# Kernel tuning notes

Hardware: AMD Instinct MI355X
Metric: run time of the kernel (lower is better)

## Reference

```python
import jax, jax.numpy as jnp
import numpy as np

K = 20  # neighbors


def _knn(x, k):
    # x: (B, C, N) -> (B, N, k) indices of k nearest neighbors (max of negative sq dist)
    inner = -2.0 * jnp.einsum('bcn,bcm->bnm', x, x)
    xx = jnp.sum(x * x, axis=1)  # (B, N)
    pd = -xx[:, :, None] - inner - xx[:, None, :]  # (B, N, N)
    return jax.lax.top_k(pd, k)[1]


def _graph_feature(x, k, dim9=False):
    # x: (B, C, N) -> (B, 2C, N, k) edge features [x_j - x_i, x_i]
    idx = _knn(x[:, 6:] if dim9 else x, k)  # (B, N, k)
    xt = jnp.transpose(x, (0, 2, 1))  # (B, N, C)
    nbr = jax.vmap(lambda t, i: t[i])(xt, idx)  # (B, N, k, C) gather
    ctr = jnp.broadcast_to(xt[:, :, None, :], nbr.shape)
    f = jnp.concatenate([nbr - ctr, ctr], axis=-1)  # (B, N, k, 2C)
    return jnp.transpose(f, (0, 3, 1, 2))


def _bn(y, p, nd):
    # inference-mode batchnorm; p = stacked (gamma, beta, mean, var) of shape (4, C)
    g, b, m, v = p
    shp = (1, -1) + (1,) * nd
    return (y - m.reshape(shp)) * (g.reshape(shp) / jnp.sqrt(v.reshape(shp) + 1e-5)) + b.reshape(shp)


def _cbr2(x, W, p):  # 1x1 conv2d + BN2d + LeakyReLU(0.2)
    return jax.nn.leaky_relu(_bn(jnp.einsum('oc,bcnk->bonk', W, x), p, 2), 0.2)


def _cbr1(x, W, p):  # 1x1 conv1d + BN1d + LeakyReLU(0.2)
    return jax.nn.leaky_relu(_bn(jnp.einsum('oc,bcn->bon', W, x), p, 1), 0.2)


def _forward(x, W1, W2, W3, W4, W5, W6, W7, W8, W9, bn1, bn2, bn3, bn4, bn5, bn6, bn7, bn8):
    N = x.shape[2]
    h = _graph_feature(x, K, dim9=True)          # (B, 12, N, K)
    h = _cbr2(h, W1, bn1)
    h = _cbr2(h, W2, bn2)
    x1 = jnp.max(h, axis=-1)                     # (B, 64, N)
    h = _graph_feature(x1, K)                    # (B, 128, N, K)
    h = _cbr2(h, W3, bn3)
    h = _cbr2(h, W4, bn4)
    x2 = jnp.max(h, axis=-1)
    h = _graph_feature(x2, K)
    h = _cbr2(h, W5, bn5)
    x3 = jnp.max(h, axis=-1)
    h = jnp.concatenate([x1, x2, x3], axis=1)    # (B, 192, N)
    h = _cbr1(h, W6, bn6)                        # (B, 1024, N)
    g = jnp.max(h, axis=-1, keepdims=True)       # global feature
    g = jnp.broadcast_to(g, (g.shape[0], g.shape[1], N))
    h = jnp.concatenate([g, x1, x2, x3], axis=1) # (B, 1216, N)
    h = _cbr1(h, W7, bn7)
    h = _cbr1(h, W8, bn8)                        # dropout is identity in eval
    return jnp.einsum('oc,bcn->bon', W9, h)      # (B, 13, N) logits


def setup_inputs() -> dict:
    key = jax.random.key(0)
    ks = jax.random.split(key, 20)
    B, C, N = 4, 6, 4096

    def w(k, o, c):
        return jax.random.normal(k, (o, c), jnp.float32) * (1.0 / np.sqrt(c))

    def bn(k, c):
        k1, k2, k3, k4 = jax.random.split(k, 4)
        g = jax.random.uniform(k1, (c,), jnp.float32, 0.5, 1.5)
        b = jax.random.normal(k2, (c,), jnp.float32) * 0.1
        m = jax.random.normal(k3, (c,), jnp.float32) * 0.1
        v = jax.random.uniform(k4, (c,), jnp.float32, 0.5, 1.5)
        return jnp.stack([g, b, m, v])

    return {
        'x': jax.random.normal(ks[0], (B, C, N), jnp.float32),
        'W1': w(ks[1], 64, 12), 'W2': w(ks[2], 64, 64), 'W3': w(ks[3], 64, 128),
        'W4': w(ks[4], 64, 64), 'W5': w(ks[5], 64, 128), 'W6': w(ks[6], 1024, 192),
        'W7': w(ks[7], 512, 1216), 'W8': w(ks[8], 256, 512), 'W9': w(ks[9], 13, 256),
        'bn1': bn(ks[10], 64), 'bn2': bn(ks[11], 64), 'bn3': bn(ks[12], 64),
        'bn4': bn(ks[13], 64), 'bn5': bn(ks[14], 64), 'bn6': bn(ks[15], 1024),
        'bn7': bn(ks[16], 512), 'bn8': bn(ks[17], 256),
    }


def reference(x, W1, W2, W3, W4, W5, W6, W7, W8, W9, bn1, bn2, bn3, bn4, bn5, bn6, bn7, bn8):
    return _forward(x, W1, W2, W3, W4, W5, W6, W7, W8, W9,
                    bn1, bn2, bn3, bn4, bn5, bn6, bn7, bn8)
```

## Files before the change

kernel.cpp:

```cpp
#include <hip/hip_runtime.h>
#include <math.h>

#define N_PTS 4096
#define BATCH 4
#define KNB 20

typedef __attribute__((ext_vector_type(8))) short short8v;
typedef __attribute__((ext_vector_type(4))) float f32x4;

__device__ __forceinline__ float lrelu(float v){ return fmaxf(v, 0.2f*v); }
__device__ __forceinline__ unsigned fenc(float f){ unsigned u=__float_as_uint(f); return (u&0x80000000u)?~u:(u|0x80000000u); }
__device__ __forceinline__ float fdec(unsigned k){ return (k&0x80000000u)?__uint_as_float(k&0x7fffffffu):__uint_as_float(~k); }

__device__ __forceinline__ unsigned pack2(float v){
  unsigned u = __float_as_uint(v);
  unsigned hi = (u + 0x7fffu + ((u>>16)&1u)) >> 16;
  float hf = __uint_as_float(hi<<16);
  unsigned u2 = __float_as_uint(v - hf);
  unsigned lo = (u2 + 0x7fffu + ((u2>>16)&1u)) >> 16;
  return (hi<<16) | lo;
}
__device__ __forceinline__ void cvt8(uint4 v0, uint4 v1, short8v& h, short8v& l){
  unsigned a0=v0.x,a1=v0.y,a2=v0.z,a3=v0.w,a4=v1.x,a5=v1.y,a6=v1.z,a7=v1.w;
  h[0]=(short)(a0>>16); l[0]=(short)(a0&0xffffu);
  h[1]=(short)(a1>>16); l[1]=(short)(a1&0xffffu);
  h[2]=(short)(a2>>16); l[2]=(short)(a2&0xffffu);
  h[3]=(short)(a3>>16); l[3]=(short)(a3&0xffffu);
  h[4]=(short)(a4>>16); l[4]=(short)(a4&0xffffu);
  h[5]=(short)(a5>>16); l[5]=(short)(a5&0xffffu);
  h[6]=(short)(a6>>16); l[6]=(short)(a6&0xffffu);
  h[7]=(short)(a7>>16); l[7]=(short)(a7&0xffffu);
}

__global__ void k_scale_rows(const float* __restrict__ W, const float* __restrict__ bn,
                             float* __restrict__ Wf, float* __restrict__ bias, int O, int C){
  int i = blockIdx.x*256 + threadIdx.x;
  if (i >= O*C) return;
  int o = i / C;
  float s = bn[o] / sqrtf(bn[3*O+o] + 1e-5f);
  Wf[i] = W[i]*s;
  if (i % C == 0) bias[o] = bn[O+o] - s*bn[2*O+o];
}

__global__ void k_pack_w(const float* __restrict__ W, int ldw, int c0,
                         const float* __restrict__ bn, int O, int C, int Opad,
                         unsigned* __restrict__ out, float* __restrict__ bias){
  int i = blockIdx.x*256 + threadIdx.x;
  if (i >= Opad*C) return;
  int o = i / C, c = i - o*C;
  float v = 0.f;
  if (o < O){
    float s = 1.f;
    if (bn != nullptr){
      s = bn[o] / sqrtf(bn[3*O+o] + 1e-5f);
      if (bias != nullptr && c == 0) bias[o] = bn[O+o] - s*bn[2*O+o];
    }
    v = W[o*ldw + c0 + c] * s;
  }
  out[i] = pack2(v);
}

__global__ void k_build_T4(const float* __restrict__ W, int ldw, const float* __restrict__ bn,
                           float* __restrict__ dst, float* __restrict__ bias,
                           int c0, int diffoff, int Csrc){
  int o = threadIdx.x, c = blockIdx.x;
  float s = bn[o] / sqrtf(bn[192+o] + 1e-5f);
  float val = 0.f;
  if (c < Csrc){
    val = W[o*ldw + c0 + c];
    if (diffoff) val = W[o*ldw + c0 + diffoff + c] - val;
    val *= s;
  }
  dst[(c>>2)*256 + o*4 + (c&3)] = val;
  if (bias != nullptr && c==0) bias[o] = bn[64+o] - s*bn[128+o];
}

__global__ void k_build_U1(const float* __restrict__ x, const float* __restrict__ W1,
                           const float* __restrict__ bn, float* __restrict__ U1){
  int o = threadIdx.x, k = blockIdx.x, b = blockIdx.y;
  float s = bn[o] / sqrtf(bn[192+o] + 1e-5f);
  float acc = 0.f;
  #pragma unroll
  for (int c=0;c<6;c++) acc += W1[o*12+c] * x[(b*6+c)*N_PTS + k];
  U1[(b*KNB+k)*64 + o] = acc*s;
}

__global__ void k_init_g(unsigned* g){ g[blockIdx.x*256+threadIdx.x] = fenc(-INFINITY); }

__global__ __launch_bounds__(256) void k_edge1(const float* __restrict__ x, const float* __restrict__ U1,
                        const float* __restrict__ W1dT4, const float* __restrict__ bf1,
                        const float* __restrict__ W2T4, const float* __restrict__ bf2,
                        float* __restrict__ x1t, unsigned* __restrict__ Xb, float* __restrict__ xx1){
  __shared__ float hb[4][KNB][64];
  int wid = threadIdx.x>>6, lane = threadIdx.x&63;
  int pt = blockIdx.x*4 + wid, b = pt>>12, n = pt&4095;
  float xv[8];
  #pragma unroll
  for (int c=0;c<6;c++) xv[c] = x[(b*6+c)*N_PTS + n];
  xv[6]=0.f; xv[7]=0.f;
  float w = bf1[lane];
  #pragma unroll
  for (int cb=0;cb<2;cb++){
    float4 wv = ((const float4*)W1dT4)[cb*64+lane];
    w = fmaf(wv.x, xv[cb*4+0], w); w = fmaf(wv.y, xv[cb*4+1], w);
    w = fmaf(wv.z, xv[cb*4+2], w); w = fmaf(wv.w, xv[cb*4+3], w);
  }
  const float* Ub = U1 + b*KNB*64;
  #pragma unroll
  for (int k=0;k<KNB;k++) hb[wid][k][lane] = lrelu(Ub[k*64+lane] + w);
  __syncthreads();
  float acc[KNB];
  #pragma unroll
  for (int k=0;k<KNB;k++) acc[k] = bf2[lane];
  for (int cb=0;cb<16;cb++){
    float4 wv = ((const float4*)W2T4)[cb*64+lane];
    #pragma unroll
    for (int k=0;k<KNB;k++){
      float4 a = *(const float4*)&hb[wid][k][cb*4];
      acc[k]=fmaf(wv.x,a.x,acc[k]); acc[k]=fmaf(wv.y,a.y,acc[k]);
      acc[k]=fmaf(wv.z,a.z,acc[k]); acc[k]=fmaf(wv.w,a.w,acc[k]);
    }
  }
  float mx = -INFINITY;
  #pragma unroll
  for (int k=0;k<KNB;k++) mx = fmaxf(mx, acc[k]);
  mx = lrelu(mx);
  x1t[(size_t)pt*64 + lane] = mx;
  Xb[((size_t)((b<<12)+n))*192 + 0 + lane] = pack2(mx);
  float sq = mx*mx;
  #pragma unroll
  for (int off=32; off; off>>=1) sq += __shfl_xor(sq, off);
  if (lane==0) xx1[pt] = sq;
}

__global__ __launch_bounds__(256) void k_uv(const float* __restrict__ xt, const float* __restrict__ WL,
    const float* __restrict__ WRd, const float* __restrict__ bf,
    float* __restrict__ Ut, float* __restrict__ Vt){
  __shared__ float xs[4][64];
  int wid = threadIdx.x>>6, lane = threadIdx.x&63;
  int pt = blockIdx.x*4 + wid;
  xs[wid][lane] = xt[(size_t)pt*64 + lane];
  __syncthreads();
  float U = 0.f, V = bf[lane];
  #pragma unroll
  for (int cb=0;cb<16;cb++){
    float4 wl = ((const float4*)WL)[cb*64+lane];
    float4 wr = ((const float4*)WRd)[cb*64+lane];
    float4 xv = *(const float4*)&xs[wid][cb*4];
    U=fmaf(wl.x,xv.x,U); U=fmaf(wl.y,xv.y,U); U=fmaf(wl.z,xv.z,U); U=fmaf(wl.w,xv.w,U);
    V=fmaf(wr.x,xv.x,V); V=fmaf(wr.y,xv.y,V); V=fmaf(wr.z,xv.z,V); V=fmaf(wr.w,xv.w,V);
  }
  Ut[(size_t)pt*64 + lane] = U;
  Vt[(size_t)pt*64 + lane] = V;
}

__global__ __launch_bounds__(256) void k_ec2(const float* __restrict__ Ut, const float* __restrict__ Vt,
    const int* __restrict__ idx, const float* __restrict__ W2T4, const float* __restrict__ bfb,
    float* __restrict__ xout, unsigned* __restrict__ Xb, float* __restrict__ xxout){
  __shared__ float H[4][KNB][64];
  int wid = threadIdx.x>>6, lane = threadIdx.x&63;
  int pt = blockIdx.x*4 + wid, b = pt>>12, n = pt&4095;
  const float* Ub = Ut + (((size_t)b)<<12)*64;
  float Vv = Vt[(size_t)pt*64 + lane];
  int mr[KNB];
  const int4* ip4 = (const int4*)(idx + (size_t)pt*KNB);
  #pragma unroll
  for (int q=0;q<5;q++){ int4 t = ip4[q]; mr[q*4+0]=t.x; mr[q*4+1]=t.y; mr[q*4+2]=t.z; mr[q*4+3]=t.w; }
  #pragma unroll
  for (int k=0;k<KNB;k++) H[wid][k][lane] = lrelu(Ub[(size_t)mr[k]*64 + lane] + Vv);
  __syncthreads();
  float acc[KNB];
  #pragma unroll
  for (int k=0;k<KNB;k++) acc[k] = bfb[lane];
  for (int cb=0;cb<16;cb++){
    float4 wv = ((const float4*)W2T4)[cb*64+lane];
    #pragma unroll
    for (int k=0;k<KNB;k++){
      float4 a = *(const float4*)&H[wid][k][cb*4];
      acc[k]=fmaf(wv.x,a.x,acc[k]); acc[k]=fmaf(wv.y,a.y,acc[k]);
      acc[k]=fmaf(wv.z,a.z,acc[k]); acc[k]=fmaf(wv.w,a.w,acc[k]);
    }
  }
  float mx = -INFINITY;
  #pragma unroll
  for (int k=0;k<KNB;k++) mx = fmaxf(mx, acc[k]);
  mx = lrelu(mx);
  xout[(size_t)pt*64 + lane] = mx;
  Xb[((size_t)((b<<12)+n))*192 + 64 + lane] = pack2(mx);
  float sq = mx*mx;
  #pragma unroll
  for (int off=32;off;off>>=1) sq += __shfl_xor(sq,off);
  if (lane==0) xxout[pt] = sq;
}

__global__ __launch_bounds__(256) void k_ec3(const float* __restrict__ Ut, const float* __restrict__ Vt,
    const int* __restrict__ idx, unsigned* __restrict__ Xb){
  int wid = threadIdx.x>>6, lane = threadIdx.x&63;
  int pt = blockIdx.x*4 + wid, b = pt>>12, n = pt&4095;
  const float* Ub = Ut + (((size_t)b)<<12)*64;
  int mr[KNB];
  const int4* ip4 = (const int4*)(idx + (size_t)pt*KNB);
  #pragma unroll
  for (int q=0;q<5;q++){ int4 t = ip4[q]; mr[q*4+0]=t.x; mr[q*4+1]=t.y; mr[q*4+2]=t.z; mr[q*4+3]=t.w; }
  float mx = -INFINITY;
  #pragma unroll
  for (int k=0;k<KNB;k++) mx = fmaxf(mx, Ub[(size_t)mr[k]*64 + lane]);
  mx = lrelu(mx + Vt[(size_t)pt*64 + lane]);
  Xb[((size_t)((b<<12)+n))*192 + 128 + lane] = pack2(mx);
}

__global__ __launch_bounds__(512) void k_knn_mfma(const unsigned* __restrict__ Xp, int coff,
        const float* __restrict__ xx, unsigned* __restrict__ pd, unsigned* __restrict__ cmax,
        int q0, int S){
  __shared__ short Ah[128][40];
  __shared__ short Al[128][40];
  __shared__ short Bh[128][40];
  __shared__ short Bl[128][40];
  int tid = threadIdx.x;
  int bx = blockIdx.x, by = blockIdx.y, bz = blockIdx.z;
  int w = tid>>6, lane = tid&63;
  int r15 = lane&15, rb = lane>>4;
  int mibase = (w&3)*32, oibase = (w>>2)*64;
  f32x4 acc[2][4];
  #pragma unroll
  for (int mi=0;mi<2;mi++)
    #pragma unroll
    for (int oi=0;oi<4;oi++) acc[mi][oi] = (f32x4){0.f,0.f,0.f,0.f};
  int srow = tid>>2, sc = (tid&3)*8;
  const unsigned* pa = Xp + ((size_t)((bz<<12) + q0 + by*128 + srow))*192 + coff + sc;
  const unsigned* pb = Xp + ((size_t)((bz<<12) + bx*128 + srow))*192 + coff + sc;
  for (int kt=0; kt<64; kt+=32){
    if (kt) __syncthreads();
    uint4 a0 = *(const uint4*)(pa+kt);
    uint4 a1 = *(const uint4*)(pa+kt+4);
    uint4 b0 = *(const uint4*)(pb+kt);
    uint4 b1 = *(const uint4*)(pb+kt+4);
    short8v h, l;
    cvt8(a0,a1,h,l);
    *(short8v*)&Ah[srow][sc] = h; *(short8v*)&Al[srow][sc] = l;
    cvt8(b0,b1,h,l);
    *(short8v*)&Bh[srow][sc] = h; *(short8v*)&Bl[srow][sc] = l;
    __syncthreads();
    short8v ah[2], al[2];
    #pragma unroll
    for (int mi=0;mi<2;mi++){
      ah[mi] = *(const short8v*)&Ah[mibase+mi*16+r15][rb*8];
      al[mi] = *(const short8v*)&Al[mibase+mi*16+r15][rb*8];
    }
    #pragma unroll
    for (int oi=0;oi<4;oi++){
      short8v bh = *(const short8v*)&Bh[oibase+oi*16+r15][rb*8];
      short8v bl = *(const short8v*)&Bl[oibase+oi*16+r15][rb*8];
      #pragma unroll
      for (int mi=0;mi<2;mi++){
        acc[mi][oi] = __builtin_amdgcn_mfma_f32_16x16x32_bf16(ah[mi], bh, acc[mi][oi], 0,0,0);
        acc[mi][oi] = __builtin_amdgcn_mfma_f32_16x16x32_bf16(ah[mi], bl, acc[mi][oi], 0,0,0);
        acc[mi][oi] = __builtin_amdgcn_mfma_f32_16x16x32_bf16(al[mi], bh, acc[mi][oi], 0,0,0);
      }
    }
  }
  float xm[4];
  #pragma unroll
  for (int oi=0;oi<4;oi++) xm[oi] = xx[(bz<<12) + bx*128 + oibase + oi*16 + r15];
  #pragma unroll
  for (int mi=0;mi<2;mi++){
    #pragma unroll
    for (int r=0;r<4;r++){
      int row = by*128 + mibase + mi*16 + rb*4 + r;
      float xn = xx[(bz<<12) + q0 + row];
      float f0 = fmaf(2.f, acc[mi][0][r], -xn) - xm[0];
      float f1 = fmaf(2.f, acc[mi][1][r], -xn) - xm[1];
      float f2 = fmaf(2.f, acc[mi][2][r], -xn) - xm[2];
      float f3 = fmaf(2.f, acc[mi][3][r], -xn) - xm[3];
      unsigned* dst = pd + ((size_t)(bz*S + row))*N_PTS + bx*128 + oibase;
      dst[ 0+r15] = fenc(f0);
      dst[16+r15] = fenc(f1);
      dst[32+r15] = fenc(f2);
      dst[48+r15] = fenc(f3);
      float m = fmaxf(fmaxf(f0,f1), fmaxf(f2,f3));
      m = fmaxf(m, __shfl_xor(m,1));
      m = fmaxf(m, __shfl_xor(m,2));
      m = fmaxf(m, __shfl_xor(m,4));
      m = fmaxf(m, __shfl_xor(m,8));
      if (r15 == 0)
        cmax[((size_t)(bz<<12) + q0 + row)*64 + bx*2 + (oibase>>6)] = fenc(m);
    }
  }
}

__device__ __forceinline__ unsigned bitsort_u32(unsigned v, int lane){
  #pragma unroll
  for (int k=2;k<=64;k<<=1){
    #pragma unroll
    for (int j=k>>1;j>0;j>>=1){
      unsigned o = (unsigned)__shfl_xor((int)v, j);
      bool takeMax = (((lane & j) != 0) == ((lane & k) == 0));
      unsigned mx = v>o?v:o, mn = v<o?v:o;
      v = takeMax ? mx : mn;
    }
  }
  return v;
}

__global__ __launch_bounds__(256,4) void k_topk20(const unsigned* __restrict__ pdbuf,
        const unsigned* __restrict__ cmax, int* __restrict__ idxout, int q0, int sshift){
  __shared__ unsigned long long cand[4][64];
  int wid = threadIdx.x>>6, lane = threadIdx.x&63;
  int gw = blockIdx.x*4 + wid;
  int S = 1 << sshift;
  int b = gw >> sshift, i = gw & (S-1);
  const unsigned* row = pdbuf + ((size_t)b*S + i)*N_PTS;
  unsigned cm = cmax[((size_t)b*N_PTS + q0 + i)*64 + lane];
  unsigned T = (unsigned)__shfl((int)bitsort_u32(cm, lane), 44);
  unsigned long long qual = __ballot(cm >= T);
  unsigned lmax = 0u;
  for (int c=0;c<64;c++){
    if (!((qual>>c)&1ull)) continue;
    unsigned vv = row[c*64 + lane];
    lmax = lmax > vv ? lmax : vv;
  }
  unsigned T2 = (unsigned)__shfl((int)bitsort_u32(lmax, lane), 44);
  int base = 0;
  unsigned long long below = (1ull<<lane) - 1ull;
  for (int c=0;c<64;c++){
    if (!((qual>>c)&1ull)) continue;
    unsigned vv = row[c*64 + lane];
    bool isc = vv >= T2;
    unsigned long long mb = __ballot(isc);
    int pos = base + __popcll(mb & below);
    if (isc && pos < 64){
      int m = c*64 + lane;
      cand[wid][pos] = (((unsigned long long)vv)<<12) | (unsigned)(4095-m);
    }
    base += __popcll(mb);
  }
  unsigned long long K;
  if (base <= 64){
    unsigned long long kv = (lane < base) ? cand[wid][lane] : 0ull;
    #pragma unroll
    for (int k=2;k<=64;k<<=1){
      #pragma unroll
      for (int j=k>>1;j>0;j>>=1){
        unsigned long long o = __shfl_xor(kv, j);
        bool takeMax = (((lane & j) != 0) == ((lane & k) == 0));
        unsigned long long mx = kv>o?kv:o, mn = kv<o?kv:o;
        kv = takeMax ? mx : mn;
      }
    }
    K = __shfl(kv, 44);
  } else {
    K = 0ull;
    for (int bb2=43; bb2>=0; --bb2){
      unsigned long long cnd = K | (1ull<<bb2);
      int lc = 0;
      for (int c=0;c<64;c++){
        if (!((qual>>c)&1ull)) continue;
        unsigned vv = row[c*64 + lane];
        int m = c*64 + lane;
        unsigned long long key = (((unsigned long long)vv)<<12) | (unsigned)(4095-m);
        if (key >= cnd) lc++;
      }
      #pragma unroll
      for (int off=32; off; off>>=1) lc += __shfl_xor(lc, off);
      if (lc >= KNB) K = cnd;
    }
  }
  int eb = 0;
  int* dst = idxout + ((size_t)b*N_PTS + (q0+i))*KNB;
  for (int c=0;c<64;c++){
    if (!((qual>>c)&1ull)) continue;
    unsigned vv = row[c*64 + lane];
    int m = c*64 + lane;
    unsigned long long key = (((unsigned long long)vv)<<12) | (unsigned)(4095-m);
    bool sel = key >= K;
    unsigned long long mb = __ballot(sel);
    int pos = eb + __popcll(mb & below);
    if (sel) dst[pos] = m;
    eb += __popcll(mb);
  }
}

template<int STORE, int RELU>
__global__ __launch_bounds__(512) void k_mgemm(const unsigned* __restrict__ Ap, int lda,
        const unsigned* __restrict__ Bp, int ldb,
        const float* __restrict__ bias, int perBatch,
        unsigned* __restrict__ Cp, int ldo, float* __restrict__ Cf,
        unsigned* __restrict__ gmax, int O, int K){
  __shared__ short Ah[128][40];
  __shared__ short Al[128][40];
  __shared__ short Bh[128][40];
  __shared__ short Bl[128][40];
  int tid = threadIdx.x;
  int bx = blockIdx.x, by = blockIdx.y, bz = blockIdx.z;
  int w = tid>>6, lane = tid&63;
  int r15 = lane&15, rb = lane>>4;
  int mibase = (w&3)*32, oibase = (w>>2)*64;
  f32x4 acc[2][4];
  #pragma unroll
  for (int mi=0;mi<2;mi++)
    #pragma unroll
    for (int oi=0;oi<4;oi++) acc[mi][oi] = (f32x4){0.f,0.f,0.f,0.f};
  int srow = tid>>2, sc = (tid&3)*8;
  const unsigned* pa = Ap + ((size_t)((bz<<12) + bx*128 + srow))*lda + sc;
  const unsigned* pb = Bp + (size_t)(by*128 + srow)*ldb + sc;
  for (int kt=0; kt<K; kt+=32){
    if (kt) __syncthreads();
    uint4 a0 = *(const uint4*)(pa+kt);
    uint4 a1 = *(const uint4*)(pa+kt+4);
    uint4 b0 = *(const uint4*)(pb+kt);
    uint4 b1 = *(const uint4*)(pb+kt+4);
    short8v h, l;
    cvt8(a0,a1,h,l);
    *(short8v*)&Ah[srow][sc] = h; *(short8v*)&Al[srow][sc] = l;
    cvt8(b0,b1,h,l);
    *(short8v*)&Bh[srow][sc] = h; *(short8v*)&Bl[srow][sc] = l;
    __syncthreads();
    short8v ah[2], al[2];
    #pragma unroll
    for (int mi=0;mi<2;mi++){
      ah[mi] = *(const short8v*)&Ah[mibase+mi*16+r15][rb*8];
      al[mi] = *(const short8v*)&Al[mibase+mi*16+r15][rb*8];
    }
    #pragma unroll
    for (int oi=0;oi<4;oi++){
      short8v bh = *(const short8v*)&Bh[oibase+oi*16+r15][rb*8];
      short8v bl = *(const short8v*)&Bl[oibase+oi*16+r15][rb*8];
      #pragma unroll
      for (int mi=0;mi<2;mi++){
        acc[mi][oi] = __builtin_amdgcn_mfma_f32_16x16x32_bf16(ah[mi], bh, acc[mi][oi], 0,0,0);
        acc[mi][oi] = __builtin_amdgcn_mfma_f32_16x16x32_bf16(ah[mi], bl, acc[mi][oi], 0,0,0);
        acc[mi][oi] = __builtin_amdgcn_mfma_f32_16x16x32_bf16(al[mi], bh, acc[mi][oi], 0,0,0);
      }
    }
  }
  #pragma unroll
  for (int oi=0;oi<4;oi++){
    int o = by*128 + oibase + oi*16 + r15;
    float bv = 0.f;
    if (bias != nullptr) bv = perBatch ? bias[bz*O + o] : bias[o];
    float cmx = -INFINITY;
    #pragma unroll
    for (int mi=0;mi<2;mi++){
      #pragma unroll
      for (int r=0;r<4;r++){
        float y = acc[mi][oi][r] + bv;
        if (RELU) y = lrelu(y);
        if (STORE==1){
          int pt = bx*128 + mibase + mi*16 + rb*4 + r;
          Cp[((size_t)((bz<<12)+pt))*ldo + o] = pack2(y);
        } else if (STORE==2){
          if (o < 13){
            int pt = bx*128 + mibase + mi*16 + rb*4 + r;
            Cf[(((size_t)(bz*13 + o))<<12) + pt] = y;
          }
        } else {
          cmx = fmaxf(cmx, y);
        }
      }
    }
    if (STORE==0){
      cmx = fmaxf(cmx, __shfl_xor(cmx,16));
      cmx = fmaxf(cmx, __shfl_xor(cmx,32));
      if (rb==0) atomicMax(&gmax[bz*1024 + o], fenc(cmx));
    }
  }
}

__global__ __launch_bounds__(256) void k_gemv7(const float* __restrict__ Wf7, const float* __restrict__ bf7,
                        const unsigned* __restrict__ g, float* __restrict__ bias7){
  int wid = threadIdx.x>>6, lane = threadIdx.x&63;
  int o = blockIdx.x*4 + wid, b = blockIdx.y;
  const float* wr = Wf7 + (size_t)o*1216;
  const unsigned* gb = g + b*1024;
  float acc = 0.f;
  for (int c = lane; c < 1024; c += 64)
    acc = fmaf(wr[c], fdec(gb[c]), acc);
  #pragma unroll
  for (int off=32; off; off>>=1) acc += __shfl_xor(acc, off);
  if (lane==0) bias7[b*512+o] = acc + bf7[o];
}

extern "C" void kernel_launch(void* const* d_in, const int* in_sizes, int n_in,
                              void* d_out, int out_size, void* d_ws, size_t ws_size,
                              hipStream_t stream){
  const float* x  = (const float*)d_in[0];
  const float* W1 = (const float*)d_in[1];
  const float* W2 = (const float*)d_in[2];
  const float* W3 = (const float*)d_in[3];
  const float* W4 = (const float*)d_in[4];
  const float* W5 = (const float*)d_in[5];
  const float* W6 = (const float*)d_in[6];
  const float* W7 = (const float*)d_in[7];
  const float* W8 = (const float*)d_in[8];
  const float* W9 = (const float*)d_in[9];
  const float* bn1 = (const float*)d_in[10];
  const float* bn2 = (const float*)d_in[11];
  const float* bn3 = (const float*)d_in[12];
  const float* bn4 = (const float*)d_in[13];
  const float* bn5 = (const float*)d_in[14];
  const float* bn6 = (const float*)d_in[15];
  const float* bn7 = (const float*)d_in[16];
  const float* bn8 = (const float*)d_in[17];

  float* ws = (float*)d_ws;
  size_t off = 0;
  auto alloc = [&](size_t nf){ float* p = ws + off; off += (nf + 63) & ~(size_t)63; return p; };
  float* Wf7 = alloc((size_t)512*1216); float* bf7 = alloc(512);
  float* bf6 = alloc(1024);
  float* bf8 = alloc(256);
  unsigned* Wb6p = (unsigned*)alloc((size_t)1024*192);
  unsigned* Wb7p = (unsigned*)alloc((size_t)512*192);
  unsigned* Wb8p = (unsigned*)alloc((size_t)256*512);
  unsigned* Wb9p = (unsigned*)alloc((size_t)128*256);
  float* W1dT4 = alloc(8*64);     float* bf1 = alloc(64);
  float* W2T4  = alloc(64*64);    float* bf2 = alloc(64);
  float* W3LT4 = alloc(64*64);    float* W3RdT4 = alloc(64*64); float* bf3 = alloc(64);
  float* W4T4  = alloc(64*64);    float* bf4 = alloc(64);
  float* W5LT4 = alloc(64*64);    float* W5RdT4 = alloc(64*64); float* bf5 = alloc(64);
  float* U1  = alloc(4*KNB*64);
  float* x1t = alloc((size_t)4*N_PTS*64);
  float* x2t = alloc((size_t)4*N_PTS*64);
  float* Ut3 = alloc((size_t)4*N_PTS*64);
  float* Vt3 = alloc((size_t)4*N_PTS*64);
  float* Ut5 = alloc((size_t)4*N_PTS*64);
  float* Vt5 = alloc((size_t)4*N_PTS*64);
  unsigned* Xb = (unsigned*)alloc((size_t)4*N_PTS*192);
  float* xx1 = alloc(4*N_PTS);
  float* xx2 = alloc(4*N_PTS);
  int* idx1 = (int*)alloc((size_t)4*N_PTS*KNB);
  int* idx2 = (int*)alloc((size_t)4*N_PTS*KNB);
  unsigned* genc = (unsigned*)alloc(4*1024);
  float* bias7 = alloc(4*512);
  unsigned* h8p = (unsigned*)alloc((size_t)4*N_PTS*256);
  unsigned* cmaxb = (unsigned*)alloc((size_t)4*N_PTS*64);
  size_t remaining = (ws_size / 4 > off) ? (ws_size / 4 - off) : 0;
  int S = 4096;
  while (S > 512 && (size_t)4*S*N_PTS + 1024 > remaining) S >>= 1;
  if (S > 1024) S = 1024;
  int sshift = 31 - __builtin_clz(S);
  unsigned* pdbuf = (unsigned*)alloc((size_t)4*S*N_PTS);
  unsigned* h7p = pdbuf;

  k_scale_rows<<<(512*1216+255)/256,256,0,stream>>>(W7, bn7, Wf7, bf7, 512, 1216);
  k_pack_w<<<(1024*192+255)/256,256,0,stream>>>(W6, 192, 0, bn6, 1024, 192, 1024, Wb6p, bf6);
  k_pack_w<<<(512*192+255)/256,256,0,stream>>>(W7, 1216, 1024, bn7, 512, 192, 512, Wb7p, nullptr);
  k_pack_w<<<(256*512+255)/256,256,0,stream>>>(W8, 512, 0, bn8, 256, 512, 256, Wb8p, bf8);
  k_pack_w<<<(128*256+255)/256,256,0,stream>>>(W9, 256, 0, nullptr, 13, 256, 128, Wb9p, nullptr);
  k_build_T4<<<8,64,0,stream>>>(W1, 12, bn1, W1dT4, bf1, 0, 6, 6);
  k_build_T4<<<64,64,0,stream>>>(W2, 64, bn2, W2T4, bf2, 0, 0, 64);
  k_build_T4<<<64,64,0,stream>>>(W3, 128, bn3, W3LT4, bf3, 0, 0, 64);
  k_build_T4<<<64,64,0,stream>>>(W3, 128, bn3, W3RdT4, nullptr, 0, 64, 64);
  k_build_T4<<<64,64,0,stream>>>(W4, 64, bn4, W4T4, bf4, 0, 0, 64);
  k_build_T4<<<64,64,0,stream>>>(W5, 128, bn5, W5LT4, bf5, 0, 0, 64);
  k_build_T4<<<64,64,0,stream>>>(W5, 128, bn5, W5RdT4, nullptr, 0, 64, 64);
  k_build_U1<<<dim3(KNB,4),64,0,stream>>>(x, W1, bn1, U1);
  k_init_g<<<16,256,0,stream>>>(genc);

  k_edge1<<<4096,256,0,stream>>>(x, U1, W1dT4, bf1, W2T4, bf2, x1t, Xb, xx1);

  int nstripe = N_PTS / S;
  for (int s=0;s<nstripe;s++){
    k_knn_mfma<<<dim3(32,S/128,4),512,0,stream>>>(Xb, 0, xx1, pdbuf, cmaxb, s*S, S);
    k_topk20<<<S,256,0,stream>>>(pdbuf, cmaxb, idx1, s*S, sshift);
  }

  k_uv<<<4096,256,0,stream>>>(x1t, W3LT4, W3RdT4, bf3, Ut3, Vt3);
  k_ec2<<<4096,256,0,stream>>>(Ut3, Vt3, idx1, W4T4, bf4, x2t, Xb, xx2);

  for (int s=0;s<nstripe;s++){
    k_knn_mfma<<<dim3(32,S/128,4),512,0,stream>>>(Xb, 64, xx2, pdbuf, cmaxb, s*S, S);
    k_topk20<<<S,256,0,stream>>>(pdbuf, cmaxb, idx2, s*S, sshift);
  }

  k_uv<<<4096,256,0,stream>>>(x2t, W5LT4, W5RdT4, bf5, Ut5, Vt5);
  k_ec3<<<4096,256,0,stream>>>(Ut5, Vt5, idx2, Xb);

  k_mgemm<0,1><<<dim3(32,8,4),512,0,stream>>>(Xb, 192, Wb6p, 192, bf6, 0, nullptr, 0, nullptr, genc, 1024, 192);
  k_gemv7<<<dim3(128,4),256,0,stream>>>(Wf7, bf7, genc, bias7);
  k_mgemm<1,1><<<dim3(32,4,4),512,0,stream>>>(Xb, 192, Wb7p, 192, bias7, 1, h7p, 512, nullptr, nullptr, 512, 192);
  k_mgemm<1,1><<<dim3(32,2,4),512,0,stream>>>(h7p, 512, Wb8p, 512, bf8, 0, h8p, 256, nullptr, nullptr, 256, 512);
  k_mgemm<2,0><<<dim3(32,1,4),512,0,stream>>>(h8p, 256, Wb9p, 256, nullptr, 0, nullptr, 0, (float*)d_out, nullptr, 13, 256);
}
```

Before: 616.5 us.

## Replace scalar edge-conv 64x64 GEMMs with split-bf16 MFMA kernel

Replaces the scalar-FMA edge-conv kernels for layers 1-2 and 3-4 with one templated kernel. It computes the second 64x64 conv through bf16 hi/lo split MFMA instructions, double-buffering the per-neighbor hidden tile in shared memory and keeping a running max. Layer 1 now precomputes a per-point V1 term in a separate kernel and uses pre-packed W2 and W4 weights. This trades the heavy FP32 FMA loops for matrix-core work, at the cost of extra split-precision MFMAs, one more launch, and a new V1 buffer. The grid is also much smaller, 256 blocks instead of 4096.

```diff
diff --git a/kernel.cpp b/kernel.cpp
--- a/kernel.cpp
+++ b/kernel.cpp
@@ -85,53 +85,20 @@
   U1[(b*KNB+k)*64 + o] = acc*s;
 }
 
+__global__ __launch_bounds__(256) void k_v1(const float* __restrict__ x, const float* __restrict__ W1,
+        const float* __restrict__ bn, float* __restrict__ V1){
+  int o = threadIdx.x&63;
+  int pt = blockIdx.x*4 + (threadIdx.x>>6);
+  int b = pt>>12, n = pt&4095;
+  float s = bn[o] / sqrtf(bn[192+o] + 1e-5f);
+  float acc = bn[64+o] - s*bn[128+o];
+  #pragma unroll
+  for (int c=0;c<6;c++)
+    acc += s*(W1[o*12+6+c]-W1[o*12+c]) * x[(b*6+c)*N_PTS + n];
+  V1[(size_t)pt*64 + o] = acc;
+}
+
 __global__ void k_init_g(unsigned* g){ g[blockIdx.x*256+threadIdx.x] = fenc(-INFINITY); }
-
-__global__ __launch_bounds__(256) void k_edge1(const float* __restrict__ x, const float* __restrict__ U1,
-                        const float* __restrict__ W1dT4, const float* __restrict__ bf1,
-                        const float* __restrict__ W2T4, const float* __restrict__ bf2,
-                        float* __restrict__ x1t, unsigned* __restrict__ Xb, float* __restrict__ xx1){
-  __shared__ float hb[4][KNB][64];
-  int wid = threadIdx.x>>6, lane = threadIdx.x&63;
-  int pt = blockIdx.x*4 + wid, b = pt>>12, n = pt&4095;
-  float xv[8];
-  #pragma unroll
-  for (int c=0;c<6;c++) xv[c] = x[(b*6+c)*N_PTS + n];
-  xv[6]=0.f; xv[7]=0.f;
-  float w = bf1[lane];
-  #pragma unroll
-  for (int cb=0;cb<2;cb++){
-    float4 wv = ((const float4*)W1dT4)[cb*64+lane];
-    w = fmaf(wv.x, xv[cb*4+0], w); w = fmaf(wv.y, xv[cb*4+1], w);
-    w = fmaf(wv.z, xv[cb*4+2], w); w = fmaf(wv.w, xv[cb*4+3], w);
-  }
-  const float* Ub = U1 + b*KNB*64;
-  #pragma unroll
-  for (int k=0;k<KNB;k++) hb[wid][k][lane] = lrelu(Ub[k*64+lane] + w);
-  __syncthreads();
-  float acc[KNB];
-  #pragma unroll
-  for (int k=0;k<KNB;k++) acc[k] = bf2[lane];
-  for (int cb=0;cb<16;cb++){
-    float4 wv = ((const float4*)W2T4)[cb*64+lane];
-    #pragma unroll
-    for (int k=0;k<KNB;k++){
-      float4 a = *(const float4*)&hb[wid][k][cb*4];
-      acc[k]=fmaf(wv.x,a.x,acc[k]); acc[k]=fmaf(wv.y,a.y,acc[k]);
-      acc[k]=fmaf(wv.z,a.z,acc[k]); acc[k]=fmaf(wv.w,a.w,acc[k]);
-    }
-  }
-  float mx = -INFINITY;
-  #pragma unroll
-  for (int k=0;k<KNB;k++) mx = fmaxf(mx, acc[k]);
-  mx = lrelu(mx);
-  x1t[(size_t)pt*64 + lane] = mx;
-  Xb[((size_t)((b<<12)+n))*192 + 0 + lane] = pack2(mx);
-  float sq = mx*mx;
-  #pragma unroll
-  for (int off=32; off; off>>=1) sq += __shfl_xor(sq, off);
-  if (lane==0) xx1[pt] = sq;
-}
 
 __global__ __launch_bounds__(256) void k_uv(const float* __restrict__ xt, const float* __restrict__ WL,
     const float* __restrict__ WRd, const float* __restrict__ bf,
@@ -154,43 +121,121 @@
   Vt[(size_t)pt*64 + lane] = V;
 }
 
-__global__ __launch_bounds__(256) void k_ec2(const float* __restrict__ Ut, const float* __restrict__ Vt,
-    const int* __restrict__ idx, const float* __restrict__ W2T4, const float* __restrict__ bfb,
-    float* __restrict__ xout, unsigned* __restrict__ Xb, float* __restrict__ xxout){
-  __shared__ float H[4][KNB][64];
-  int wid = threadIdx.x>>6, lane = threadIdx.x&63;
-  int pt = blockIdx.x*4 + wid, b = pt>>12, n = pt&4095;
-  const float* Ub = Ut + (((size_t)b)<<12)*64;
-  float Vv = Vt[(size_t)pt*64 + lane];
+template<int GATHER>
+__global__ __launch_bounds__(256) void k_edgemm(const float* __restrict__ Ut,
+    const float* __restrict__ Vt, const int* __restrict__ idx,
+    const unsigned* __restrict__ Wp, const float* __restrict__ bf,
+    float* __restrict__ xout, unsigned* __restrict__ Xb, int coff,
+    float* __restrict__ xxout){
+  __shared__ short Hh[2][64][72];
+  __shared__ short Hl[2][64][72];
+  int tid = threadIdx.x;
+  int b = blockIdx.z, p0 = blockIdx.x*64;
+  int w = tid>>6, lane = tid&63, r15 = lane&15, rb = lane>>4;
+  int ptl = tid>>2, c0 = (tid&3)*16;
+  size_t ptg = ((size_t)b<<12) + p0 + ptl;
+  float v[16];
+  #pragma unroll
+  for (int q=0;q<4;q++){
+    float4 t = *(const float4*)&Vt[ptg*64 + c0 + q*4];
+    v[q*4+0]=t.x; v[q*4+1]=t.y; v[q*4+2]=t.z; v[q*4+3]=t.w;
+  }
   int mr[KNB];
-  const int4* ip4 = (const int4*)(idx + (size_t)pt*KNB);
-  #pragma unroll
-  for (int q=0;q<5;q++){ int4 t = ip4[q]; mr[q*4+0]=t.x; mr[q*4+1]=t.y; mr[q*4+2]=t.z; mr[q*4+3]=t.w; }
-  #pragma unroll
-  for (int k=0;k<KNB;k++) H[wid][k][lane] = lrelu(Ub[(size_t)mr[k]*64 + lane] + Vv);
-  __syncthreads();
-  float acc[KNB];
-  #pragma unroll
-  for (int k=0;k<KNB;k++) acc[k] = bfb[lane];
-  for (int cb=0;cb<16;cb++){
-    float4 wv = ((const float4*)W2T4)[cb*64+lane];
-    #pragma unroll
-    for (int k=0;k<KNB;k++){
-      float4 a = *(const float4*)&H[wid][k][cb*4];
-      acc[k]=fmaf(wv.x,a.x,acc[k]); acc[k]=fmaf(wv.y,a.y,acc[k]);
-      acc[k]=fmaf(wv.z,a.z,acc[k]); acc[k]=fmaf(wv.w,a.w,acc[k]);
-    }
-  }
-  float mx = -INFINITY;
-  #pragma unroll
-  for (int k=0;k<KNB;k++) mx = fmaxf(mx, acc[k]);
-  mx = lrelu(mx);
-  xout[(size_t)pt*64 + lane] = mx;
-  Xb[((size_t)((b<<12)+n))*192 + 64 + lane] = pack2(mx);
-  float sq = mx*mx;
-  #pragma unroll
-  for (int off=32;off;off>>=1) sq += __shfl_xor(sq,off);
-  if (lane==0) xxout[pt] = sq;
+  if (GATHER){
+    const int4* ip4 = (const int4*)(idx + ptg*KNB);
+    #pragma unroll
+    for (int q=0;q<5;q++){ int4 t=ip4[q]; mr[q*4+0]=t.x; mr[q*4+1]=t.y; mr[q*4+2]=t.z; mr[q*4+3]=t.w; }
+  }
+  short8v wh[4][2], wl[4][2];
+  #pragma unroll
+  for (int oi=0;oi<4;oi++)
+    #pragma unroll
+    for (int ks=0;ks<2;ks++){
+      const unsigned* pw = Wp + (size_t)(oi*16+r15)*64 + ks*32 + rb*8;
+      uint4 w0 = *(const uint4*)pw, w1 = *(const uint4*)(pw+4);
+      cvt8(w0,w1,wh[oi][ks],wl[oi][ks]);
+    }
+  f32x4 rmax[4];
+  #pragma unroll
+  for (int oi=0;oi<4;oi++) rmax[oi]=(f32x4){-INFINITY,-INFINITY,-INFINITY,-INFINITY};
+  float uc[16], un[16];
+  {
+    const float* ur = GATHER ? (Ut + ((((size_t)b)<<12) + mr[0])*64 + c0)
+                             : (Ut + ((size_t)b*KNB + 0)*64 + c0);
+    #pragma unroll
+    for (int q=0;q<4;q++){
+      float4 t = *(const float4*)(ur + q*4);
+      uc[q*4+0]=t.x; uc[q*4+1]=t.y; uc[q*4+2]=t.z; uc[q*4+3]=t.w;
+    }
+  }
+  for (int k=0;k<KNB;k++){
+    int buf = k&1;
+    #pragma unroll
+    for (int q=0;q<2;q++){
+      short8v hh, hl;
+      #pragma unroll
+      for (int e=0;e<8;e++){
+        unsigned pk = pack2(lrelu(uc[q*8+e] + v[q*8+e]));
+        hh[e]=(short)(pk>>16); hl[e]=(short)(pk&0xffffu);
+      }
+      *(short8v*)&Hh[buf][ptl][c0+q*8] = hh;
+      *(short8v*)&Hl[buf][ptl][c0+q*8] = hl;
+    }
+    if (k+1 < KNB){
+      const float* ur = GATHER ? (Ut + ((((size_t)b)<<12) + mr[k+1])*64 + c0)
+                               : (Ut + ((size_t)b*KNB + (k+1))*64 + c0);
+      #pragma unroll
+      for (int q=0;q<4;q++){
+        float4 t = *(const float4*)(ur + q*4);
+        un[q*4+0]=t.x; un[q*4+1]=t.y; un[q*4+2]=t.z; un[q*4+3]=t.w;
+      }
+    }
+    __syncthreads();
+    f32x4 acc[4];
+    #pragma unroll
+    for (int oi=0;oi<4;oi++) acc[oi]=(f32x4){0.f,0.f,0.f,0.f};
+    #pragma unroll
+    for (int ks=0;ks<2;ks++){
+      short8v ah = *(const short8v*)&Hh[buf][w*16+r15][ks*32+rb*8];
+      short8v al = *(const short8v*)&Hl[buf][w*16+r15][ks*32+rb*8];
+      #pragma unroll
+      for (int oi=0;oi<4;oi++){
+        acc[oi] = __builtin_amdgcn_mfma_f32_16x16x32_bf16(ah, wh[oi][ks], acc[oi], 0,0,0);
+        acc[oi] = __builtin_amdgcn_mfma_f32_16x16x32_bf16(ah, wl[oi][ks], acc[oi], 0,0,0);
+        acc[oi] = __builtin_amdgcn_mfma_f32_16x16x32_bf16(al, wh[oi][ks], acc[oi], 0,0,0);
+      }
+    }
+    #pragma unroll
+    for (int oi=0;oi<4;oi++)
+      #pragma unroll
+      for (int r=0;r<4;r++) rmax[oi][r] = fmaxf(rmax[oi][r], acc[oi][r]);
+    if (k+1 < KNB){
+      #pragma unroll
+      for (int e=0;e<16;e++) uc[e]=un[e];
+    }
+  }
+  float xs[4] = {0.f,0.f,0.f,0.f};
+  #pragma unroll
+  for (int oi=0;oi<4;oi++){
+    int o = oi*16 + r15;
+    float bv = bf[o];
+    #pragma unroll
+    for (int r=0;r<4;r++){
+      float y = lrelu(rmax[oi][r] + bv);
+      size_t pg = ((size_t)b<<12) + p0 + w*16 + rb*4 + r;
+      if (xout) xout[pg*64 + o] = y;
+      Xb[pg*192 + coff + o] = pack2(y);
+      xs[r] += y*y;
+    }
+  }
+  if (xxout){
+    #pragma unroll
+    for (int r=0;r<4;r++){
+      float s = xs[r];
+      s += __shfl_xor(s,1); s += __shfl_xor(s,2); s += __shfl_xor(s,4); s += __shfl_xor(s,8);
+      if (r15==0) xxout[((size_t)b<<12) + p0 + w*16 + rb*4 + r] = s;
+    }
+  }
 }
 
 __global__ __launch_bounds__(256) void k_ec3(const float* __restrict__ Ut, const float* __restrict__ Vt,
@@ -508,16 +553,18 @@
   float* Wf7 = alloc((size_t)512*1216); float* bf7 = alloc(512);
   float* bf6 = alloc(1024);
   float* bf8 = alloc(256);
+  float* bf2 = alloc(64);
+  float* bf4 = alloc(64);
+  unsigned* Wb2p = (unsigned*)alloc((size_t)64*64);
+  unsigned* Wb4p = (unsigned*)alloc((size_t)64*64);
   unsigned* Wb6p = (unsigned*)alloc((size_t)1024*192);
   unsigned* Wb7p = (unsigned*)alloc((size_t)512*192);
   unsigned* Wb8p = (unsigned*)alloc((size_t)256*512);
   unsigned* Wb9p = (unsigned*)alloc((size_t)128*256);
-  float* W1dT4 = alloc(8*64);     float* bf1 = alloc(64);
-  float* W2T4  = alloc(64*64);    float* bf2 = alloc(64);
   float* W3LT4 = alloc(64*64);    float* W3RdT4 = alloc(64*64); float* bf3 = alloc(64);
-  float* W4T4  = alloc(64*64);    float* bf4 = alloc(64);
   float* W5LT4 = alloc(64*64);    float* W5RdT4 = alloc(64*64); float* bf5 = alloc(64);
   float* U1  = alloc(4*KNB*64);
+  float* V1  = alloc((size_t)4*N_PTS*64);
   float* x1t = alloc((size_t)4*N_PTS*64);
   float* x2t = alloc((size_t)4*N_PTS*64);
   float* Ut3 = alloc((size_t)4*N_PTS*64);
@@ -542,21 +589,21 @@
   unsigned* h7p = pdbuf;
 
   k_scale_rows<<<(512*1216+255)/256,256,0,stream>>>(W7, bn7, Wf7, bf7, 512, 1216);
+  k_pack_w<<<(64*64+255)/256,256,0,stream>>>(W2, 64, 0, bn2, 64, 64, 64, Wb2p, bf2);
+  k_pack_w<<<(64*64+255)/256,256,0,stream>>>(W4, 64, 0, bn4, 64, 64, 64, Wb4p, bf4);
   k_pack_w<<<(1024*192+255)/256,256,0,stream>>>(W6, 192, 0, bn6, 1024, 192, 1024, Wb6p, bf6);
   k_pack_w<<<(512*192+255)/256,256,0,stream>>>(W7, 1216, 1024, bn7, 512, 192, 512, Wb7p, nullptr);
   k_pack_w<<<(256*512+255)/256,256,0,stream>>>(W8, 512, 0, bn8, 256, 512, 256, Wb8p, bf8);
   k_pack_w<<<(128*256+255)/256,256,0,stream>>>(W9, 256, 0, nullptr, 13, 256, 128, Wb9p, nullptr);
-  k_build_T4<<<8,64,0,stream>>>(W1, 12, bn1, W1dT4, bf1, 0, 6, 6);
-  k_build_T4<<<64,64,0,stream>>>(W2, 64, bn2, W2T4, bf2, 0, 0, 64);
   k_build_T4<<<64,64,0,stream>>>(W3, 128, bn3, W3LT4, bf3, 0, 0, 64);
   k_build_T4<<<64,64,0,stream>>>(W3, 128, bn3, W3RdT4, nullptr, 0, 64, 64);
-  k_build_T4<<<64,64,0,stream>>>(W4, 64, bn4, W4T4, bf4, 0, 0, 64);
   k_build_T4<<<64,64,0,stream>>>(W5, 128, bn5, W5LT4, bf5, 0, 0, 64);
   k_build_T4<<<64,64,0,stream>>>(W5, 128, bn5, W5RdT4, nullptr, 0, 64, 64);
   k_build_U1<<<dim3(KNB,4),64,0,stream>>>(x, W1, bn1, U1);
+  k_v1<<<4096,256,0,stream>>>(x, W1, bn1, V1);
   k_init_g<<<16,256,0,stream>>>(genc);
 
-  k_edge1<<<4096,256,0,stream>>>(x, U1, W1dT4, bf1, W2T4, bf2, x1t, Xb, xx1);
+  k_edgemm<0><<<dim3(64,1,4),256,0,stream>>>(U1, V1, nullptr, Wb2p, bf2, x1t, Xb, 0, xx1);
 
   int nstripe = N_PTS / S;
   for (int s=0;s<nstripe;s++){
@@ -565,7 +612,7 @@
   }
 
   k_uv<<<4096,256,0,stream>>>(x1t, W3LT4, W3RdT4, bf3, Ut3, Vt3);
-  k_ec2<<<4096,256,0,stream>>>(Ut3, Vt3, idx1, W4T4, bf4, x2t, Xb, xx2);
+  k_edgemm<1><<<dim3(64,1,4),256,0,stream>>>(Ut3, Vt3, idx1, Wb4p, bf4, x2t, Xb, 64, xx2);
 
   for (int s=0;s<nstripe;s++){
     k_knn_mfma<<<dim3(32,S/128,4),512,0,stream>>>(Xb, 64, xx2, pdbuf, cmaxb, s*S, S);
```

After: 561.3 us (median of 2 runs). -8.9%, faster.
